# Kernel tuning notes

Hardware: AMD Instinct MI355X
Metric: run time of the kernel (lower is better)

The kernel has to match this reference:

```python
import jax, jax.numpy as jnp
import numpy as np

N, E, D_IN, D_HID, D_OUT = 10000, 160000, 512, 512, 256


def gcn_conv(x, W, src, tgt, n):
    # GCNConv, bias=False: out = D^{-1/2} (A+I) D^{-1/2} (x @ W)
    xw = x @ W                                              # [n, d_out]
    ones = jnp.ones(src.shape[0], dtype=xw.dtype)
    deg = jax.ops.segment_sum(ones, tgt, num_segments=n)    # in-degree incl. self-loop
    dinv = jnp.where(deg > 0, jax.lax.rsqrt(deg), 0.0)
    norm = dinv[src] * dinv[tgt]                            # [e]
    msg = norm[:, None] * xw[src]                           # gather + scale, [e, d_out]
    return jax.ops.segment_sum(msg, tgt, num_segments=n)    # scatter-add to targets


def setup_inputs() -> dict:
    key = jax.random.key(0)
    k1, k2, k3, k4 = jax.random.split(key, 4)
    x = jax.random.normal(k1, (N, D_IN), dtype=jnp.float32)
    edge_index = jax.random.randint(k2, (2, E), 0, N, dtype=jnp.int32)
    W1 = jax.random.normal(k3, (D_IN, D_HID), dtype=jnp.float32) * (1.0 / np.sqrt(D_IN))
    W2 = jax.random.normal(k4, (D_HID, D_OUT), dtype=jnp.float32) * (1.0 / np.sqrt(D_HID))
    return {"x": x, "edge_index": edge_index, "W1": W1, "W2": W2}


def reference(x, edge_index, W1, W2):
    n = x.shape[0]
    loops = jnp.arange(n, dtype=edge_index.dtype)
    src = jnp.concatenate([edge_index[0], loops])  # add self-loops once, reuse both layers
    tgt = jnp.concatenate([edge_index[1], loops])
    h = gcn_conv(x, W1, src, tgt, n)
    h = h ** 2                                     # square activation
    # F.dropout with training=False (eval / inference reference) is identity
    return gcn_conv(h, W2, src, tgt, n)
```

## Files before the change

kernel.cpp:

```cpp
#include <hip/hip_runtime.h>
#include <stdint.h>

typedef __attribute__((ext_vector_type(8))) short bf16x8;
typedef __attribute__((ext_vector_type(4))) short bf16x4;
typedef __attribute__((ext_vector_type(4))) float f32x4;

#define DEGCAP 64

static __device__ __forceinline__ unsigned short f2bf(float f) {
    unsigned int u = __float_as_uint(f);
    u = u + 0x7FFFu + ((u >> 16) & 1u);
    return (unsigned short)(u >> 16);
}
static __device__ __forceinline__ float bf2f(short b) {
    return __uint_as_float(((unsigned int)(unsigned short)b) << 16);
}

#define GLD_LDS16(g, l) __builtin_amdgcn_global_load_lds( \
    (const __attribute__((address_space(1))) uint32_t*)(g), \
    (__attribute__((address_space(3))) uint32_t*)(l), 16, 0, 0)


__global__ __launch_bounds__(256) void k_setup(
    const int* __restrict__ src, const int* __restrict__ tgt,
    int* __restrict__ cnt, int* __restrict__ esrc, int E,
    const float* __restrict__ x, unsigned short* __restrict__ xb, int total4,
    const float* __restrict__ W1, unsigned short* __restrict__ w1t,
    const float* __restrict__ W2, unsigned short* __restrict__ w2t)
{
    const int bid = blockIdx.x;
    const int tid = threadIdx.x;
    if (bid < 625) {
        int e = bid * 256 + tid;
        if (e < E) {
            int t = tgt[e];
            int pos = atomicAdd(&cnt[t], 1);
            if (pos < DEGCAP) esrc[(size_t)t * DEGCAP + pos] = src[e];
        }
    } else if (bid < 5625) {
        int i = (bid - 625) * 256 + tid;
        if (i < total4) {
            float4 v = ((const float4*)x)[i];
            ushort4 o;
            o.x = f2bf(v.x); o.y = f2bf(v.y); o.z = f2bf(v.z); o.w = f2bf(v.w);
            ((ushort4*)xb)[i] = o;
        }
    } else if (bid < 6649) {
        int idx = (bid - 5625) * 256 + tid;
        int k = idx >> 9, n = idx & 511;
        w1t[(size_t)n * 512 + k] = f2bf(W1[idx]);
    } else {
        int idx = (bid - 6649) * 256 + tid;
        int k = idx >> 8, n = idx & 255;
        w2t[(size_t)n * 512 + k] = f2bf(W2[idx]);
    }
}


template<bool SCALE_ROW>
__global__ __launch_bounds__(256) void k_gemm(
    const short* __restrict__ A,
    const short* __restrict__ Bt,
    const int* __restrict__ cnt,
    unsigned short* __restrict__ C,
    int M, int N, int K, int ncol, int q, int r)
{
    __shared__ char smem[24576];
    char* smA = smem;
    char* smB = smem + 8192;

    const int orig = blockIdx.x;
    const int xcd = orig & 7, loc = orig >> 3;
    const int wg = (xcd < r ? xcd * (q + 1) : r * (q + 1) + (xcd - r) * q) + loc;
    const int rowbase = (wg / ncol) * 64;
    const int colbase = (wg % ncol) * 128;

    const int tid  = threadIdx.x;
    const int lane = tid & 63;
    const int wave = tid >> 6;

    const int lrow = (lane >> 3);
    const int scol = ((lane & 7) ^ lrow) << 3;
    const int rA0 = wave * 8 + lrow;
    int gA0 = rowbase + rA0;          if (gA0 >= M) gA0 = M - 1;
    int gA1 = rowbase + rA0 + 32;     if (gA1 >= M) gA1 = M - 1;
    const size_t offA0 = (size_t)gA0 * K + scol;
    const size_t offA1 = (size_t)gA1 * K + scol;
    size_t offB[4];
#pragma unroll
    for (int c = 0; c < 4; ++c)
        offB[c] = (size_t)(colbase + c * 32 + rA0) * K + scol;

    char* const dA0 = smA + wave * 1024;
    char* const dA1 = smA + 4096 + wave * 1024;
    char* dB[4];
#pragma unroll
    for (int c = 0; c < 4; ++c) dB[c] = smB + c * 4096 + wave * 1024;

    const int wr = (wave >> 1) * 32;
    const int wc = (wave & 1) * 64;
    const int fr = lane & 15;
    const int fs = lane >> 4;

    f32x4 acc[2][4];
#pragma unroll
    for (int m = 0; m < 2; ++m)
#pragma unroll
        for (int n = 0; n < 4; ++n)
            acc[m][n] = (f32x4){0.f, 0.f, 0.f, 0.f};

    for (int k0 = 0; k0 < K; k0 += 64) {
        GLD_LDS16(A + offA0 + k0, dA0);
        GLD_LDS16(A + offA1 + k0, dA1);
#pragma unroll
        for (int c = 0; c < 4; ++c)
            GLD_LDS16(Bt + offB[c] + k0, dB[c]);
        __syncthreads();

        bf16x8 a[2][2], b[4][2];
#pragma unroll
        for (int m = 0; m < 2; ++m)
#pragma unroll
            for (int ks = 0; ks < 2; ++ks) {
                int rr = wr + m * 16 + fr;
                int s = ks * 4 + fs;
                a[m][ks] = *(const bf16x8*)(smA + rr * 128 + ((s ^ (rr & 7)) << 4));
            }
#pragma unroll
        for (int n = 0; n < 4; ++n)
#pragma unroll
            for (int ks = 0; ks < 2; ++ks) {
                int rr = wc + n * 16 + fr;
                int s = ks * 4 + fs;
                b[n][ks] = *(const bf16x8*)(smB + rr * 128 + ((s ^ (rr & 7)) << 4));
            }
#pragma unroll
        for (int m = 0; m < 2; ++m)
#pragma unroll
            for (int n = 0; n < 4; ++n)
#pragma unroll
                for (int ks = 0; ks < 2; ++ks)
                    acc[m][n] = __builtin_amdgcn_mfma_f32_16x16x32_bf16(
                        a[m][ks], b[n][ks], acc[m][n], 0, 0, 0);
        __syncthreads();
    }

    const int orow0 = rowbase + wr + fs * 4;
    const int ocol0 = colbase + wc + fr;
#pragma unroll
    for (int m = 0; m < 2; ++m)
#pragma unroll
        for (int i = 0; i < 4; ++i) {
            int row = orow0 + m * 16 + i;
            if (row < M) {
                float sc = SCALE_ROW ? rsqrtf((float)(cnt[row] + 1)) : 1.0f;
#pragma unroll
                for (int n = 0; n < 4; ++n)
                    C[(size_t)row * N + ocol0 + n * 16] = f2bf(sc * acc[m][n][i]);
            }
        }
}


__global__ __launch_bounds__(256) void k_agg1(
    const unsigned short* __restrict__ xwb,
    const int* __restrict__ cnt, const int* __restrict__ esrc,
    unsigned short* __restrict__ hb, int Nn)
{
    const int t = blockIdx.x * 4 + (threadIdx.x >> 6);
    if (t >= Nn) return;
    const int lane = threadIdx.x & 63;
    int deg = cnt[t]; if (deg > DEGCAP) deg = DEGCAP;
    const float dt = rsqrtf((float)(deg + 1));
    const int* eb = esrc + (size_t)t * DEGCAP;

    float acc[8];
    bf16x8 v = *(const bf16x8*)(xwb + (size_t)t * 512 + lane * 8);
#pragma unroll
    for (int j = 0; j < 8; ++j) acc[j] = bf2f(v[j]);

    int e = 0;
    for (; e + 7 < deg; e += 8) {
        int s[8];
#pragma unroll
        for (int j = 0; j < 8; ++j) s[j] = eb[e + j];
        bf16x8 u[8];
#pragma unroll
        for (int j = 0; j < 8; ++j)
            u[j] = *(const bf16x8*)(xwb + (size_t)s[j] * 512 + lane * 8);
#pragma unroll
        for (int j = 0; j < 8; ++j)
#pragma unroll
            for (int c = 0; c < 8; ++c) acc[c] += bf2f(u[j][c]);
    }
    for (; e + 3 < deg; e += 4) {
        int s[4];
#pragma unroll
        for (int j = 0; j < 4; ++j) s[j] = eb[e + j];
        bf16x8 u[4];
#pragma unroll
        for (int j = 0; j < 4; ++j)
            u[j] = *(const bf16x8*)(xwb + (size_t)s[j] * 512 + lane * 8);
#pragma unroll
        for (int j = 0; j < 4; ++j)
#pragma unroll
            for (int c = 0; c < 8; ++c) acc[c] += bf2f(u[j][c]);
    }
    for (; e < deg; ++e) {
        int s = eb[e];
        bf16x8 u = *(const bf16x8*)(xwb + (size_t)s * 512 + lane * 8);
#pragma unroll
        for (int c = 0; c < 8; ++c) acc[c] += bf2f(u[c]);
    }

    bf16x8 o;
#pragma unroll
    for (int c = 0; c < 8; ++c) {
        float pre = dt * acc[c];
        o[c] = (short)f2bf(dt * pre * pre);
    }
    *(bf16x8*)(hb + (size_t)t * 512 + lane * 8) = o;
}

__global__ __launch_bounds__(256) void k_agg2(
    const unsigned short* __restrict__ xwb,
    const int* __restrict__ cnt, const int* __restrict__ esrc,
    float* __restrict__ out, int Nn)
{
    const int t = blockIdx.x * 4 + (threadIdx.x >> 6);
    if (t >= Nn) return;
    const int lane = threadIdx.x & 63;
    int deg = cnt[t]; if (deg > DEGCAP) deg = DEGCAP;
    const float dt = rsqrtf((float)(deg + 1));
    const int* eb = esrc + (size_t)t * DEGCAP;

    float acc[4];
    bf16x4 v = *(const bf16x4*)(xwb + (size_t)t * 256 + lane * 4);
#pragma unroll
    for (int j = 0; j < 4; ++j) acc[j] = bf2f(v[j]);

    int e = 0;
    for (; e + 7 < deg; e += 8) {
        int s[8];
#pragma unroll
        for (int j = 0; j < 8; ++j) s[j] = eb[e + j];
        bf16x4 u[8];
#pragma unroll
        for (int j = 0; j < 8; ++j)
            u[j] = *(const bf16x4*)(xwb + (size_t)s[j] * 256 + lane * 4);
#pragma unroll
        for (int j = 0; j < 8; ++j)
#pragma unroll
            for (int c = 0; c < 4; ++c) acc[c] += bf2f(u[j][c]);
    }
    for (; e + 3 < deg; e += 4) {
        int s[4];
#pragma unroll
        for (int j = 0; j < 4; ++j) s[j] = eb[e + j];
        bf16x4 u[4];
#pragma unroll
        for (int j = 0; j < 4; ++j)
            u[j] = *(const bf16x4*)(xwb + (size_t)s[j] * 256 + lane * 4);
#pragma unroll
        for (int j = 0; j < 4; ++j)
#pragma unroll
            for (int c = 0; c < 4; ++c) acc[c] += bf2f(u[j][c]);
    }
    for (; e < deg; ++e) {
        int s = eb[e];
        bf16x4 u = *(const bf16x4*)(xwb + (size_t)s * 256 + lane * 4);
#pragma unroll
        for (int c = 0; c < 4; ++c) acc[c] += bf2f(u[c]);
    }

    float4 rout;
    rout.x = dt * acc[0]; rout.y = dt * acc[1];
    rout.z = dt * acc[2]; rout.w = dt * acc[3];
    ((float4*)(out + (size_t)t * 256))[lane] = rout;
}


extern "C" void kernel_launch(void* const* d_in, const int* in_sizes, int n_in,
                              void* d_out, int out_size, void* d_ws, size_t ws_size,
                              hipStream_t stream) {
    const float* x   = (const float*)d_in[0];
    const int*  eidx = (const int*)d_in[1];
    const float* W1  = (const float*)d_in[2];
    const float* W2  = (const float*)d_in[3];
    float* out = (float*)d_out;

    const int DIN = 512, DHID = 512, DOUT = 256;
    const int Nn = in_sizes[0] / DIN;
    const int E  = in_sizes[1] / 2;
    const int* src = eidx;
    const int* tgt = eidx + E;

    char* ws = (char*)d_ws;
    size_t off = 0;
    auto alloc = [&](size_t bytes) -> char* {
        off = (off + 255) & ~(size_t)255;
        char* p = ws + off;
        off += bytes;
        return p;
    };

    int* cnt  = (int*)alloc((size_t)Nn * 4);
    int* esrc = (int*)alloc((size_t)Nn * DEGCAP * 4);
    unsigned short* xb   = (unsigned short*)alloc((size_t)Nn * DIN * 2);
    unsigned short* w1t  = (unsigned short*)alloc((size_t)DIN * DHID * 2);
    unsigned short* w2t  = (unsigned short*)alloc((size_t)DHID * DOUT * 2);
    unsigned short* xwb  = (unsigned short*)alloc((size_t)Nn * DHID * 2);
    unsigned short* hb   = (unsigned short*)alloc((size_t)Nn * DHID * 2);
    unsigned short* xw2b = (unsigned short*)alloc((size_t)Nn * DOUT * 2);

    (void)hipMemsetAsync(cnt, 0, (size_t)Nn * 4, stream);

    const int total4 = Nn * DIN / 4;
    k_setup<<<7161, 256, 0, stream>>>(src, tgt, cnt, esrc, E,
                                      x, xb, total4, W1, w1t, W2, w2t);

    {
        const int nrow = (Nn + 63) / 64, ncol = DHID / 128;
        const int nwg = nrow * ncol;
        k_gemm<true><<<nwg, 256, 0, stream>>>(
            (const short*)xb, (const short*)w1t, cnt, xwb,
            Nn, DHID, DIN, ncol, nwg >> 3, nwg & 7);
    }
    k_agg1<<<(Nn + 3) / 4, 256, 0, stream>>>(xwb, cnt, esrc, hb, Nn);

    {
        const int nrow = (Nn + 63) / 64, ncol = DOUT / 128;
        const int nwg = nrow * ncol;
        k_gemm<false><<<nwg, 256, 0, stream>>>(
            (const short*)hb, (const short*)w2t, cnt, xw2b,
            Nn, DOUT, DHID, ncol, nwg >> 3, nwg & 7);
    }
    k_agg2<<<(Nn + 3) / 4, 256, 0, stream>>>(xw2b, cnt, esrc, out, Nn);
}
```

Baseline: 83.12 us.

## Store GEMM outputs column-blocked and split aggregation across feature blocks

The GEMM epilogue now writes its output in 128-column panels (panel-major layout). Both aggregation kernels launch one block per feature panel, so each wave gathers a contiguous 256-byte slice of a neighbor row per edge instead of a whole row. The per-panel working set is smaller, which should improve L2 hit rates on the random gathers. The cost is that the edge-index and degree reads are repeated once per panel, each lane does narrower 4-byte loads, and the final output uses nontemporal stores.

```diff
diff --git a/kernel.cpp b/kernel.cpp
--- a/kernel.cpp
+++ b/kernel.cpp
@@ -2,8 +2,8 @@
 #include <stdint.h>
 
 typedef __attribute__((ext_vector_type(8))) short bf16x8;
-typedef __attribute__((ext_vector_type(4))) short bf16x4;
 typedef __attribute__((ext_vector_type(4))) float f32x4;
+typedef __attribute__((ext_vector_type(2))) float f32x2;
 
 #define DEGCAP 64
 
@@ -14,6 +14,12 @@
 }
 static __device__ __forceinline__ float bf2f(short b) {
     return __uint_as_float(((unsigned int)(unsigned short)b) << 16);
+}
+static __device__ __forceinline__ float bflo(unsigned int v) {
+    return __uint_as_float(v << 16);
+}
+static __device__ __forceinline__ float bfhi(unsigned int v) {
+    return __uint_as_float(v & 0xffff0000u);
 }
 
 #define GLD_LDS16(g, l) __builtin_amdgcn_global_load_lds( \
@@ -145,8 +151,9 @@
         __syncthreads();
     }
 
+    unsigned short* Cq = C + (size_t)(colbase >> 7) * M * 128;
     const int orow0 = rowbase + wr + fs * 4;
-    const int ocol0 = colbase + wc + fr;
+    const int ocol0 = wc + fr;
 #pragma unroll
     for (int m = 0; m < 2; ++m)
 #pragma unroll
@@ -156,127 +163,114 @@
                 float sc = SCALE_ROW ? rsqrtf((float)(cnt[row] + 1)) : 1.0f;
 #pragma unroll
                 for (int n = 0; n < 4; ++n)
-                    C[(size_t)row * N + ocol0 + n * 16] = f2bf(sc * acc[m][n][i]);
+                    Cq[(size_t)row * 128 + ocol0 + n * 16] = f2bf(sc * acc[m][n][i]);
             }
         }
 }
 
 
 __global__ __launch_bounds__(256) void k_agg1(
-    const unsigned short* __restrict__ xwb,
+    const unsigned int* __restrict__ xwb,
     const int* __restrict__ cnt, const int* __restrict__ esrc,
-    unsigned short* __restrict__ hb, int Nn)
+    unsigned int* __restrict__ hb, int Nn)
 {
-    const int t = blockIdx.x * 4 + (threadIdx.x >> 6);
+    const int blk = blockIdx.x & 3;
+    const int t = (blockIdx.x >> 2) * 4 + (threadIdx.x >> 6);
     if (t >= Nn) return;
     const int lane = threadIdx.x & 63;
     int deg = cnt[t]; if (deg > DEGCAP) deg = DEGCAP;
     const float dt = rsqrtf((float)(deg + 1));
     const int* eb = esrc + (size_t)t * DEGCAP;
-
-    float acc[8];
-    bf16x8 v = *(const bf16x8*)(xwb + (size_t)t * 512 + lane * 8);
-#pragma unroll
-    for (int j = 0; j < 8; ++j) acc[j] = bf2f(v[j]);
+    const unsigned int* xq = xwb + (size_t)blk * Nn * 64 + lane;
+
+    float a0, a1;
+    {
+        unsigned int v = xq[(size_t)t * 64];
+        a0 = bflo(v); a1 = bfhi(v);
+    }
 
     int e = 0;
     for (; e + 7 < deg; e += 8) {
         int s[8];
 #pragma unroll
         for (int j = 0; j < 8; ++j) s[j] = eb[e + j];
-        bf16x8 u[8];
-#pragma unroll
-        for (int j = 0; j < 8; ++j)
-            u[j] = *(const bf16x8*)(xwb + (size_t)s[j] * 512 + lane * 8);
-#pragma unroll
-        for (int j = 0; j < 8; ++j)
-#pragma unroll
-            for (int c = 0; c < 8; ++c) acc[c] += bf2f(u[j][c]);
+        unsigned int u[8];
+#pragma unroll
+        for (int j = 0; j < 8; ++j) u[j] = xq[(size_t)s[j] * 64];
+#pragma unroll
+        for (int j = 0; j < 8; ++j) { a0 += bflo(u[j]); a1 += bfhi(u[j]); }
     }
     for (; e + 3 < deg; e += 4) {
         int s[4];
 #pragma unroll
         for (int j = 0; j < 4; ++j) s[j] = eb[e + j];
-        bf16x8 u[4];
-#pragma unroll
-        for (int j = 0; j < 4; ++j)
-            u[j] = *(const bf16x8*)(xwb + (size_t)s[j] * 512 + lane * 8);
-#pragma unroll
-        for (int j = 0; j < 4; ++j)
-#pragma unroll
-            for (int c = 0; c < 8; ++c) acc[c] += bf2f(u[j][c]);
+        unsigned int u[4];
+#pragma unroll
+        for (int j = 0; j < 4; ++j) u[j] = xq[(size_t)s[j] * 64];
+#pragma unroll
+        for (int j = 0; j < 4; ++j) { a0 += bflo(u[j]); a1 += bfhi(u[j]); }
     }
     for (; e < deg; ++e) {
-        int s = eb[e];
-        bf16x8 u = *(const bf16x8*)(xwb + (size_t)s * 512 + lane * 8);
-#pragma unroll
-        for (int c = 0; c < 8; ++c) acc[c] += bf2f(u[c]);
-    }
-
-    bf16x8 o;
-#pragma unroll
-    for (int c = 0; c < 8; ++c) {
-        float pre = dt * acc[c];
-        o[c] = (short)f2bf(dt * pre * pre);
-    }
-    *(bf16x8*)(hb + (size_t)t * 512 + lane * 8) = o;
+        unsigned int u = xq[(size_t)eb[e] * 64];
+        a0 += bflo(u); a1 += bfhi(u);
+    }
+
+    float p0 = dt * a0, p1 = dt * a1;
+    p0 = dt * p0 * p0;
+    p1 = dt * p1 * p1;
+    hb[(size_t)t * 256 + blk * 64 + lane] =
+        ((unsigned int)f2bf(p1) << 16) | (unsigned int)f2bf(p0);
 }
 
 __global__ __launch_bounds__(256) void k_agg2(
-    const unsigned short* __restrict__ xwb,
+    const unsigned int* __restrict__ xwb,
     const int* __restrict__ cnt, const int* __restrict__ esrc,
     float* __restrict__ out, int Nn)
 {
-    const int t = blockIdx.x * 4 + (threadIdx.x >> 6);
+    const int blk = blockIdx.x & 1;
+    const int t = (blockIdx.x >> 1) * 4 + (threadIdx.x >> 6);
     if (t >= Nn) return;
     const int lane = threadIdx.x & 63;
     int deg = cnt[t]; if (deg > DEGCAP) deg = DEGCAP;
     const float dt = rsqrtf((float)(deg + 1));
     const int* eb = esrc + (size_t)t * DEGCAP;
-
-    float acc[4];
-    bf16x4 v = *(const bf16x4*)(xwb + (size_t)t * 256 + lane * 4);
-#pragma unroll
-    for (int j = 0; j < 4; ++j) acc[j] = bf2f(v[j]);
+    const unsigned int* xq = xwb + (size_t)blk * Nn * 64 + lane;
+
+    float a0, a1;
+    {
+        unsigned int v = xq[(size_t)t * 64];
+        a0 = bflo(v); a1 = bfhi(v);
+    }
 
     int e = 0;
     for (; e + 7 < deg; e += 8) {
         int s[8];
 #pragma unroll
         for (int j = 0; j < 8; ++j) s[j] = eb[e + j];
-        bf16x4 u[8];
-#pragma unroll
-        for (int j = 0; j < 8; ++j)
-            u[j] = *(const bf16x4*)(xwb + (size_t)s[j] * 256 + lane * 4);
-#pragma unroll
-        for (int j = 0; j < 8; ++j)
-#pragma unroll
-            for (int c = 0; c < 4; ++c) acc[c] += bf2f(u[j][c]);
+        unsigned int u[8];
+#pragma unroll
+        for (int j = 0; j < 8; ++j) u[j] = xq[(size_t)s[j] * 64];
+#pragma unroll
+        for (int j = 0; j < 8; ++j) { a0 += bflo(u[j]); a1 += bfhi(u[j]); }
     }
     for (; e + 3 < deg; e += 4) {
         int s[4];
 #pragma unroll
         for (int j = 0; j < 4; ++j) s[j] = eb[e + j];
-        bf16x4 u[4];
-#pragma unroll
-        for (int j = 0; j < 4; ++j)
-            u[j] = *(const bf16x4*)(xwb + (size_t)s[j] * 256 + lane * 4);
-#pragma unroll
-        for (int j = 0; j < 4; ++j)
-#pragma unroll
-            for (int c = 0; c < 4; ++c) acc[c] += bf2f(u[j][c]);
+        unsigned int u[4];
+#pragma unroll
+        for (int j = 0; j < 4; ++j) u[j] = xq[(size_t)s[j] * 64];
+#pragma unroll
+        for (int j = 0; j < 4; ++j) { a0 += bflo(u[j]); a1 += bfhi(u[j]); }
     }
     for (; e < deg; ++e) {
-        int s = eb[e];
-        bf16x4 u = *(const bf16x4*)(xwb + (size_t)s * 256 + lane * 4);
-#pragma unroll
-        for (int c = 0; c < 4; ++c) acc[c] += bf2f(u[c]);
-    }
-
-    float4 rout;
-    rout.x = dt * acc[0]; rout.y = dt * acc[1];
-    rout.z = dt * acc[2]; rout.w = dt * acc[3];
-    ((float4*)(out + (size_t)t * 256))[lane] = rout;
+        unsigned int u = xq[(size_t)eb[e] * 64];
+        a0 += bflo(u); a1 += bfhi(u);
+    }
+
+    f32x2 r;
+    r[0] = dt * a0; r[1] = dt * a1;
+    __builtin_nontemporal_store(r, (f32x2*)(out + (size_t)t * 256 + blk * 128 + lane * 2));
 }
 
 
@@ -326,7 +320,8 @@
             (const short*)xb, (const short*)w1t, cnt, xwb,
             Nn, DHID, DIN, ncol, nwg >> 3, nwg & 7);
     }
-    k_agg1<<<(Nn + 3) / 4, 256, 0, stream>>>(xwb, cnt, esrc, hb, Nn);
+    k_agg1<<<4 * ((Nn + 3) / 4), 256, 0, stream>>>(
+        (const unsigned int*)xwb, cnt, esrc, (unsigned int*)hb, Nn);
 
     {
         const int nrow = (Nn + 63) / 64, ncol = DOUT / 128;
@@ -335,5 +330,6 @@
             (const short*)hb, (const short*)w2t, cnt, xw2b,
             Nn, DOUT, DHID, ncol, nwg >> 3, nwg & 7);
     }
-    k_agg2<<<(Nn + 3) / 4, 256, 0, stream>>>(xw2b, cnt, esrc, out, Nn);
-}
+    k_agg2<<<2 * ((Nn + 3) / 4), 256, 0, stream>>>(
+        (const unsigned int*)xw2b, cnt, esrc, out, Nn);
+}
```

Measured after the change: 80.61 us. 3.0% less time.
